# Optimization experiments

Measured on AMD Instinct MI355X. Metric: run time of the kernel, lower is better.

Reference implementation:

```python
import jax, jax.numpy as jnp
import numpy as np

B, G, C = 16384, 7, 30  # batch, 7x7 grid, 2*5 box params + 20 classes


def setup_inputs() -> dict:
    key = jax.random.key(0)
    k1, k2 = jax.random.split(key)
    pred = jax.random.uniform(k1, (B, G, G, C), dtype=jnp.float32)
    labels = jax.random.uniform(k2, (B, G, G, C), dtype=jnp.float32)
    # channel 0 of labels is the object-presence indicator (==1 where a gt box exists)
    labels = labels.at[..., 0].set((labels[..., 0] > 0.7).astype(jnp.float32))
    return {"pred": pred, "labels": labels}


def _corners(box):
    # box channels: [conf, x, y, w, h]
    x, y, w, h = box[..., 1], box[..., 2], box[..., 3], box[..., 4]
    return x - 0.5 * w, x + 0.5 * w, y - 0.5 * h, y + 0.5 * h  # left,right,top,bottom


def _iou(b1, b2):
    l1, r1, t1, bt1 = _corners(b1)
    l2, r2, t2, bt2 = _corners(b2)
    in_h = jnp.minimum(bt1, bt2) - jnp.maximum(t1, t2)
    in_w = jnp.minimum(r1, r2) - jnp.maximum(l1, l2)
    inter = jnp.where((in_h < 0) | (in_w < 0), 0.0, in_h * in_w)
    area1 = (bt1 - t1) * (r1 - l1)
    area2 = (bt2 - t2) * (r2 - l2)
    return inter / (area1 + area2 - inter)


def reference(pred, labels):
    mask = labels[..., 0]                     # [B,7,7] object indicator (0/1)
    box1 = pred[..., 0:5]
    box2 = pred[..., 5:10]
    gt = labels[..., 0:5]
    iou1 = _iou(box1, gt)
    iou2 = _iou(box2, gt)
    best = iou1 >= iou2                       # responsible box per cell
    sel = jnp.where(best[..., None], box1, box2)
    iou_max = jnp.where(best, iou1, iou2)
    iou_min = jnp.where(best, iou2, iou1)
    center = 5.0 * ((sel[..., 1] - gt[..., 1]) ** 2 + (sel[..., 2] - gt[..., 2]) ** 2)
    wh = 5.0 * ((jnp.sqrt(sel[..., 3]) - jnp.sqrt(gt[..., 3])) ** 2
                + (jnp.sqrt(sel[..., 4]) - jnp.sqrt(gt[..., 4])) ** 2)
    cls = jnp.sum((pred[..., 10:] - labels[..., 10:]) ** 2, axis=-1)

    def msum(x):
        return jnp.sum(x * mask)

    # [center, wh, obj_conf, noobj_conf, classification]
    return jnp.stack([msum(center), msum(wh), msum(iou_max), msum(iou_min), msum(cls)])
```

## Files before the change

kernel.cpp:

```cpp
#include <hip/hip_runtime.h>
#include <stdint.h>

#define NCH    30
#define TPW    64
#define TILE   64
#define TWORDS (TILE * NCH)
#define TF4    (2 * TWORDS / 4)
#define LOADS  (TF4 / TPW)
#define NBLK   1280

__device__ __forceinline__ float iou_f(float x1, float y1, float w1, float h1,
                                       float x2, float y2, float w2, float h2) {
    float l1 = x1 - 0.5f * w1, r1 = x1 + 0.5f * w1;
    float t1 = y1 - 0.5f * h1, b1 = y1 + 0.5f * h1;
    float l2 = x2 - 0.5f * w2, r2 = x2 + 0.5f * w2;
    float t2 = y2 - 0.5f * h2, b2 = y2 + 0.5f * h2;
    float in_h = fminf(b1, b2) - fmaxf(t1, t2);
    float in_w = fminf(r1, r2) - fmaxf(l1, l2);
    float inter = (in_h < 0.f || in_w < 0.f) ? 0.f : in_h * in_w;
    float a1 = (b1 - t1) * (r1 - l1);
    float a2 = (b2 - t2) * (r2 - l2);
    return inter / (a1 + a2 - inter);
}

__device__ __forceinline__ void cell_loss(const float* __restrict__ pp,
                                          const float* __restrict__ lp,
                                          float& v0, float& v1, float& v2,
                                          float& v3, float& v4) {
    const float2 l01 = *(const float2*)(lp);
    const float mask = l01.x;
    if (mask == 0.f) return;

    const float2 l23 = *(const float2*)(lp + 2);
    const float2 l45 = *(const float2*)(lp + 4);
    const float gx = l01.y, gy = l23.x, gw = l23.y, gh = l45.x;

    const float2 p01 = *(const float2*)(pp);
    const float2 p23 = *(const float2*)(pp + 2);
    const float2 p45 = *(const float2*)(pp + 4);
    const float2 p67 = *(const float2*)(pp + 6);
    const float2 p89 = *(const float2*)(pp + 8);

    const float i1 = iou_f(p01.y, p23.x, p23.y, p45.x, gx, gy, gw, gh);
    const float i2 = iou_f(p67.x, p67.y, p89.x, p89.y, gx, gy, gw, gh);
    const bool best = (i1 >= i2);
    const float sx = best ? p01.y : p67.x;
    const float sy = best ? p23.x : p67.y;
    const float sw = best ? p23.y : p89.x;
    const float sh = best ? p45.x : p89.y;
    const float imax = best ? i1 : i2;
    const float imin = best ? i2 : i1;

    const float center = 5.f * ((sx - gx) * (sx - gx) + (sy - gy) * (sy - gy));
    const float dw = sqrtf(sw) - sqrtf(gw);
    const float dh = sqrtf(sh) - sqrtf(gh);
    const float wh = 5.f * (dw * dw + dh * dh);

    float cls = 0.f;
#pragma unroll
    for (int k = 0; k < 10; ++k) {
        const float2 pd = *(const float2*)(pp + 10 + 2 * k);
        const float2 ld = *(const float2*)(lp + 10 + 2 * k);
        const float dx = pd.x - ld.x;
        const float dy = pd.y - ld.y;
        cls += dx * dx + dy * dy;
    }

    v0 += center * mask;
    v1 += wh * mask;
    v2 += imax * mask;
    v3 += imin * mask;
    v4 += cls * mask;
}

__global__ __launch_bounds__(TPW) void yolo_partial(const float* __restrict__ pred,
                                                    const float* __restrict__ lab,
                                                    float* __restrict__ partial,
                                                    int n_cells) {
    __shared__ float s[4 * TWORDS];
    const int lane = threadIdx.x;
    const int bid = blockIdx.x;
    const int NB = gridDim.x;
    const int nt = n_cells / TILE;

    float v0 = 0.f, v1 = 0.f, v2 = 0.f, v3 = 0.f, v4 = 0.f;

    float4 r[LOADS];

    auto LOAD = [&](int tile) {
#pragma unroll
        for (int i = 0; i < LOADS; ++i) {
            const int idx = i * TPW + lane;
            const float* src = (idx < TWORDS / 4)
                ? (pred + (size_t)tile * TWORDS + (size_t)idx * 4)
                : (lab  + (size_t)tile * TWORDS + (size_t)(idx - TWORDS / 4) * 4);
            r[i] = *(const float4*)src;
        }
    };
    auto WRITE = [&](float* buf) {
#pragma unroll
        for (int i = 0; i < LOADS; ++i) {
            const int idx = i * TPW + lane;
            *(float4*)(buf + (size_t)idx * 4) = r[i];
        }
    };

    float* A = s;
    float* B = s + 2 * TWORDS;

    if (bid < nt) {
        LOAD(bid);
        WRITE(A);
        if (bid + NB < nt) LOAD(bid + NB);

        for (int t = bid; t < nt; t += NB) {
            cell_loss(A + lane * NCH, A + TWORDS + lane * NCH, v0, v1, v2, v3, v4);

            if (t + NB < nt) {
                WRITE(B);
                if (t + 2 * NB < nt) LOAD(t + 2 * NB);
            }
            float* tmp = A; A = B; B = tmp;
        }
    }

    const int rem_start = nt * TILE;
    if (bid == 0 && rem_start < n_cells) {
        for (int c = rem_start + lane; c < n_cells; c += TPW) {
            cell_loss(pred + (size_t)c * NCH, lab + (size_t)c * NCH,
                      v0, v1, v2, v3, v4);
        }
    }

#pragma unroll
    for (int off = 32; off > 0; off >>= 1) {
        v0 += __shfl_down(v0, off);
        v1 += __shfl_down(v1, off);
        v2 += __shfl_down(v2, off);
        v3 += __shfl_down(v3, off);
        v4 += __shfl_down(v4, off);
    }
    if (lane == 0) {
        float* p = partial + (size_t)bid * 5;
        p[0] = v0; p[1] = v1; p[2] = v2; p[3] = v3; p[4] = v4;
    }
}

__global__ __launch_bounds__(256) void final_reduce(const float* __restrict__ partial,
                                                    float* __restrict__ out,
                                                    int n_blocks) {
    __shared__ float red[5][4];
    const int tid = threadIdx.x;
    float v0 = 0.f, v1 = 0.f, v2 = 0.f, v3 = 0.f, v4 = 0.f;
    for (int b = tid; b < n_blocks; b += 256) {
        const float* p = partial + (size_t)b * 5;
        v0 += p[0]; v1 += p[1]; v2 += p[2]; v3 += p[3]; v4 += p[4];
    }
#pragma unroll
    for (int off = 32; off > 0; off >>= 1) {
        v0 += __shfl_down(v0, off);
        v1 += __shfl_down(v1, off);
        v2 += __shfl_down(v2, off);
        v3 += __shfl_down(v3, off);
        v4 += __shfl_down(v4, off);
    }
    const int wave = tid >> 6;
    const int lane = tid & 63;
    if (lane == 0) {
        red[0][wave] = v0;
        red[1][wave] = v1;
        red[2][wave] = v2;
        red[3][wave] = v3;
        red[4][wave] = v4;
    }
    __syncthreads();
    if (tid < 5) {
        float sacc = 0.f;
#pragma unroll
        for (int w = 0; w < 4; ++w) sacc += red[tid][w];
        out[tid] = sacc;
    }
}

extern "C" void kernel_launch(void* const* d_in, const int* in_sizes, int n_in,
                              void* d_out, int out_size, void* d_ws, size_t ws_size,
                              hipStream_t stream) {
    const float* pred = (const float*)d_in[0];
    const float* lab  = (const float*)d_in[1];
    float* out = (float*)d_out;
    float* partial = (float*)d_ws;

    const int n_cells = in_sizes[0] / NCH;

    hipLaunchKernelGGL(yolo_partial, dim3(NBLK), dim3(TPW), 0, stream,
                       pred, lab, partial, n_cells);
    hipLaunchKernelGGL(final_reduce, dim3(1), dim3(256), 0, stream,
                       partial, out, NBLK);
}
```

Before: 238.8 us.

## Replace register double-buffering with chunked loads and doubled grid

Removes the software pipeline that prefetched the next tile into registers and kept two shared-memory buffers. Each tile is now loaded directly in two smaller register chunks (8 then 7 float4 per lane), written to a single LDS buffer, and consumed at once. This halves LDS and register use per block and doubles the block count, so latency is hidden by more resident waves rather than by explicit prefetch. The cost is that each tile's load latency is no longer overlapped within a wave, and the two chunks are issued as two separate load rounds.

After: 209.6 us. -12.2%, faster.

```diff
diff --git a/kernel.cpp b/kernel.cpp
--- a/kernel.cpp
+++ b/kernel.cpp
@@ -5,9 +5,11 @@
 #define TPW    64
 #define TILE   64
 #define TWORDS (TILE * NCH)
-#define TF4    (2 * TWORDS / 4)
-#define LOADS  (TF4 / TPW)
-#define NBLK   1280
+#define NF4    (2 * TWORDS / 4)
+#define LOADS  (NF4 / TPW)
+#define C0     8
+#define C1     7
+#define NBLK   2560
 
 __device__ __forceinline__ float iou_f(float x1, float y1, float w1, float h1,
                                        float x2, float y2, float w2, float h2) {
@@ -77,7 +79,7 @@
                                                     const float* __restrict__ lab,
                                                     float* __restrict__ partial,
                                                     int n_cells) {
-    __shared__ float s[4 * TWORDS];
+    __shared__ float s[2 * TWORDS];
     const int lane = threadIdx.x;
     const int bid = blockIdx.x;
     const int NB = gridDim.x;
@@ -85,43 +87,43 @@
 
     float v0 = 0.f, v1 = 0.f, v2 = 0.f, v3 = 0.f, v4 = 0.f;
 
-    float4 r[LOADS];
-
-    auto LOAD = [&](int tile) {
-#pragma unroll
-        for (int i = 0; i < LOADS; ++i) {
-            const int idx = i * TPW + lane;
-            const float* src = (idx < TWORDS / 4)
-                ? (pred + (size_t)tile * TWORDS + (size_t)idx * 4)
-                : (lab  + (size_t)tile * TWORDS + (size_t)(idx - TWORDS / 4) * 4);
-            r[i] = *(const float4*)src;
+    for (int t = bid; t < nt; t += NB) {
+        const size_t base = (size_t)t * TWORDS;
+
+        {
+            float4 ra[C0];
+#pragma unroll
+            for (int i = 0; i < C0; ++i) {
+                const int idx = i * TPW + lane;
+                const float* src = (idx < TWORDS / 4)
+                    ? (pred + base + (size_t)idx * 4)
+                    : (lab  + base + (size_t)(idx - TWORDS / 4) * 4);
+                ra[i] = *(const float4*)src;
+            }
+#pragma unroll
+            for (int i = 0; i < C0; ++i) {
+                const int idx = i * TPW + lane;
+                *(float4*)(s + (size_t)idx * 4) = ra[i];
+            }
         }
-    };
-    auto WRITE = [&](float* buf) {
-#pragma unroll
-        for (int i = 0; i < LOADS; ++i) {
-            const int idx = i * TPW + lane;
-            *(float4*)(buf + (size_t)idx * 4) = r[i];
+        {
+            float4 rb[C1];
+#pragma unroll
+            for (int i = 0; i < C1; ++i) {
+                const int idx = (C0 + i) * TPW + lane;
+                const float* src = (idx < TWORDS / 4)
+                    ? (pred + base + (size_t)idx * 4)
+                    : (lab  + base + (size_t)(idx - TWORDS / 4) * 4);
+                rb[i] = *(const float4*)src;
+            }
+#pragma unroll
+            for (int i = 0; i < C1; ++i) {
+                const int idx = (C0 + i) * TPW + lane;
+                *(float4*)(s + (size_t)idx * 4) = rb[i];
+            }
         }
-    };
-
-    float* A = s;
-    float* B = s + 2 * TWORDS;
-
-    if (bid < nt) {
-        LOAD(bid);
-        WRITE(A);
-        if (bid + NB < nt) LOAD(bid + NB);
-
-        for (int t = bid; t < nt; t += NB) {
-            cell_loss(A + lane * NCH, A + TWORDS + lane * NCH, v0, v1, v2, v3, v4);
-
-            if (t + NB < nt) {
-                WRITE(B);
-                if (t + 2 * NB < nt) LOAD(t + 2 * NB);
-            }
-            float* tmp = A; A = B; B = tmp;
-        }
+
+        cell_loss(s + lane * NCH, s + TWORDS + lane * NCH, v0, v1, v2, v3, v4);
     }
 
     const int rem_start = nt * TILE;
```

## Load labels first and fetch only pred float4s for cells with objects

Applied to the files above, without the earlier changes.

Each tile now loads the label data into shared memory first, builds a ballot bitmask of cells whose object indicator is nonzero, and then loads only the pred float4 chunks that overlap those cells. Since roughly 70% of cells carry no object, this targets the pred read bandwidth. The register double-buffering pipeline is replaced by a simple load, sync, compute loop with 128-thread blocks and a block-level reduction. The trade-off is lost load/compute overlap, extra barriers, and partial-cacheline reads that may not save much DRAM traffic, since 30-float cells straddle 128-byte lines.

After: 215.4 us. 9.8% less time.

```diff
diff --git a/kernel.cpp b/kernel.cpp
--- a/kernel.cpp
+++ b/kernel.cpp
@@ -1,13 +1,12 @@
 #include <hip/hip_runtime.h>
 #include <stdint.h>
 
-#define NCH    30
-#define TPW    64
-#define TILE   64
-#define TWORDS (TILE * NCH)
-#define TF4    (2 * TWORDS / 4)
-#define LOADS  (TF4 / TPW)
-#define NBLK   1280
+#define NCH   30
+#define TPB   128
+#define TILE  128
+#define TW    (TILE * NCH)
+#define TF4   (TW / 4)
+#define NBLK  1280
 
 __device__ __forceinline__ float iou_f(float x1, float y1, float w1, float h1,
                                        float x2, float y2, float w2, float h2) {
@@ -73,60 +72,67 @@
     v4 += cls * mask;
 }
 
-__global__ __launch_bounds__(TPW) void yolo_partial(const float* __restrict__ pred,
+__global__ __launch_bounds__(TPB) void yolo_partial(const float* __restrict__ pred,
                                                     const float* __restrict__ lab,
                                                     float* __restrict__ partial,
                                                     int n_cells) {
-    __shared__ float s[4 * TWORDS];
-    const int lane = threadIdx.x;
-    const int bid = blockIdx.x;
-    const int NB = gridDim.x;
-    const int nt = n_cells / TILE;
+    __shared__ float sl[TW];
+    __shared__ float sp[TW];
+    __shared__ unsigned long long sbits[TPB / 64];
+    __shared__ float red[5][TPB / 64];
+
+    const int tid  = threadIdx.x;
+    const int wave = tid >> 6;
+    const int lane = tid & 63;
+    const int bid  = blockIdx.x;
+    const int NB   = gridDim.x;
+    const int nt   = n_cells / TILE;
 
     float v0 = 0.f, v1 = 0.f, v2 = 0.f, v3 = 0.f, v4 = 0.f;
 
-    float4 r[LOADS];
-
-    auto LOAD = [&](int tile) {
-#pragma unroll
-        for (int i = 0; i < LOADS; ++i) {
-            const int idx = i * TPW + lane;
-            const float* src = (idx < TWORDS / 4)
-                ? (pred + (size_t)tile * TWORDS + (size_t)idx * 4)
-                : (lab  + (size_t)tile * TWORDS + (size_t)(idx - TWORDS / 4) * 4);
-            r[i] = *(const float4*)src;
+    for (int t = bid; t < nt; t += NB) {
+        const size_t base = (size_t)t * TW;
+
+#pragma unroll
+        for (int i = 0; i < 8; ++i) {
+            const int idx = i * TPB + tid;
+            if (idx < TF4)
+                *(float4*)(sl + (size_t)idx * 4) =
+                    *(const float4*)(lab + base + (size_t)idx * 4);
         }
-    };
-    auto WRITE = [&](float* buf) {
-#pragma unroll
-        for (int i = 0; i < LOADS; ++i) {
-            const int idx = i * TPW + lane;
-            *(float4*)(buf + (size_t)idx * 4) = r[i];
+        __syncthreads();
+
+        const float my_mask = sl[tid * NCH];
+        const unsigned long long bits = __ballot(my_mask != 0.f);
+        if (lane == 0) sbits[wave] = bits;
+        __syncthreads();
+
+        const unsigned long long b0 = sbits[0];
+        const unsigned long long b1 = sbits[1];
+
+#pragma unroll
+        for (int i = 0; i < 8; ++i) {
+            const int idx = i * TPB + tid;
+            if (idx < TF4) {
+                const int f0 = idx * 4;
+                const int c0 = f0 / NCH;
+                const int c1 = (f0 + 3) / NCH;
+                const bool n0 = (c0 < 64) ? ((b0 >> c0) & 1ull) : ((b1 >> (c0 - 64)) & 1ull);
+                const bool n1 = (c1 < 64) ? ((b0 >> c1) & 1ull) : ((b1 >> (c1 - 64)) & 1ull);
+                if (n0 || n1)
+                    *(float4*)(sp + (size_t)idx * 4) =
+                        *(const float4*)(pred + base + (size_t)idx * 4);
+            }
         }
-    };
-
-    float* A = s;
-    float* B = s + 2 * TWORDS;
-
-    if (bid < nt) {
-        LOAD(bid);
-        WRITE(A);
-        if (bid + NB < nt) LOAD(bid + NB);
-
-        for (int t = bid; t < nt; t += NB) {
-            cell_loss(A + lane * NCH, A + TWORDS + lane * NCH, v0, v1, v2, v3, v4);
-
-            if (t + NB < nt) {
-                WRITE(B);
-                if (t + 2 * NB < nt) LOAD(t + 2 * NB);
-            }
-            float* tmp = A; A = B; B = tmp;
-        }
+        __syncthreads();
+
+        cell_loss(sp + tid * NCH, sl + tid * NCH, v0, v1, v2, v3, v4);
+        __syncthreads();
     }
 
     const int rem_start = nt * TILE;
     if (bid == 0 && rem_start < n_cells) {
-        for (int c = rem_start + lane; c < n_cells; c += TPW) {
+        for (int c = rem_start + tid; c < n_cells; c += TPB) {
             cell_loss(pred + (size_t)c * NCH, lab + (size_t)c * NCH,
                       v0, v1, v2, v3, v4);
         }
@@ -141,8 +147,18 @@
         v4 += __shfl_down(v4, off);
     }
     if (lane == 0) {
-        float* p = partial + (size_t)bid * 5;
-        p[0] = v0; p[1] = v1; p[2] = v2; p[3] = v3; p[4] = v4;
+        red[0][wave] = v0;
+        red[1][wave] = v1;
+        red[2][wave] = v2;
+        red[3][wave] = v3;
+        red[4][wave] = v4;
+    }
+    __syncthreads();
+    if (tid < 5) {
+        float sacc = 0.f;
+#pragma unroll
+        for (int w = 0; w < TPB / 64; ++w) sacc += red[tid][w];
+        partial[(size_t)bid * 5 + tid] = sacc;
     }
 }
 
@@ -192,7 +208,7 @@
 
     const int n_cells = in_sizes[0] / NCH;
 
-    hipLaunchKernelGGL(yolo_partial, dim3(NBLK), dim3(TPW), 0, stream,
+    hipLaunchKernelGGL(yolo_partial, dim3(NBLK), dim3(TPB), 0, stream,
                        pred, lab, partial, n_cells);
     hipLaunchKernelGGL(final_reduce, dim3(1), dim3(256), 0, stream,
                        partial, out, NBLK);
```
